# Optimization experiments

Hardware: AMD Instinct MI355X
Metric: run time of the kernel (lower is better)

## Reference

```python
import jax, jax.numpy as jnp
import numpy as np

B, S, H = 2, 2048, 4096
NH, NKV, HD = 32, 8, 128
N_REP = NH // NKV
ROPE_BASE = 10000.0
NEG_INF = -1e9


def setup_inputs() -> dict:
    key = jax.random.key(0)
    k1, k2, k3, k4, k5 = jax.random.split(key, 5)
    hidden_states = jax.random.normal(k1, (B, S, H), dtype=jnp.float32)
    # standard prefill positions 0..S-1 for each batch row
    position_ids = jnp.tile(jnp.arange(S, dtype=jnp.int64)[None, :], (B, 1))
    # additive causal mask, broadcastable over batch and heads
    causal = jnp.tril(jnp.ones((S, S), dtype=bool))
    attention_mask = jnp.where(causal, 0.0, NEG_INF).astype(jnp.float32)[None, None]
    scale = 0.02
    Wq = jax.random.normal(k2, (H, NH * HD), dtype=jnp.float32) * scale
    Wk = jax.random.normal(k3, (H, NKV * HD), dtype=jnp.float32) * scale
    Wv = jax.random.normal(k4, (H, NKV * HD), dtype=jnp.float32) * scale
    Wo = jax.random.normal(k5, (NH * HD, H), dtype=jnp.float32) * scale
    return {"hidden_states": hidden_states, "position_ids": position_ids,
            "attention_mask": attention_mask, "Wq": Wq, "Wk": Wk, "Wv": Wv, "Wo": Wo}


def _rope_cos_sin(position_ids):
    # inv_freq: [HD/2]
    inv_freq = 1.0 / (ROPE_BASE ** (jnp.arange(0, HD, 2, dtype=jnp.float32) / HD))
    freqs = position_ids.astype(jnp.float32)[:, :, None] * inv_freq[None, None, :]  # [B,S,HD/2]
    emb = jnp.concatenate([freqs, freqs], axis=-1)  # [B,S,HD]
    # unsqueeze head dim (unsqueeze_dim=1)
    return jnp.cos(emb)[:, None], jnp.sin(emb)[:, None]  # [B,1,S,HD]


def _rotate_half(x):
    x1, x2 = jnp.split(x, 2, axis=-1)
    return jnp.concatenate([-x2, x1], axis=-1)


def reference(hidden_states, position_ids, attention_mask, Wq, Wk, Wv, Wo):
    b, s, _ = hidden_states.shape
    q = jnp.einsum('bsh,hd->bsd', hidden_states, Wq).reshape(b, s, NH, HD).transpose(0, 2, 1, 3)
    k = jnp.einsum('bsh,hd->bsd', hidden_states, Wk).reshape(b, s, NKV, HD).transpose(0, 2, 1, 3)
    v = jnp.einsum('bsh,hd->bsd', hidden_states, Wv).reshape(b, s, NKV, HD).transpose(0, 2, 1, 3)

    cos, sin = _rope_cos_sin(position_ids)  # [B,1,S,HD]
    q = q * cos + _rotate_half(q) * sin
    k = k * cos + _rotate_half(k) * sin

    # GQA: repeat each kv head N_REP times consecutively -> [B,NH,S,HD]
    k = jnp.repeat(k, N_REP, axis=1)
    v = jnp.repeat(v, N_REP, axis=1)

    scores = jnp.einsum('bhqd,bhkd->bhqk', q, k) / np.sqrt(HD).astype(np.float32)
    scores = scores + attention_mask
    attn = jax.nn.softmax(scores, axis=-1)
    out = jnp.einsum('bhqk,bhkd->bhqd', attn, v)  # [B,NH,S,HD]
    out = out.transpose(0, 2, 1, 3).reshape(b, s, NH * HD)
    return out @ Wo
```

## Files before the change

kernel.cpp:

```cpp
#include <hip/hip_runtime.h>
#include <hip/hip_bf16.h>
#include <stdint.h>
#include <math.h>

#define S_LEN 2048
#define NHEAD 32
#define NKVH  8
#define HDIM  128
#define HID   4096

typedef __attribute__((ext_vector_type(4))) float f32x4;
typedef __attribute__((ext_vector_type(8))) short s16x8;
typedef __attribute__((ext_vector_type(4))) short s16x4;

__device__ __forceinline__ float bf2f(ushort u){
  union { float f; uint32_t i; } c; c.i = ((uint32_t)u) << 16; return c.f;
}
__device__ __forceinline__ ushort f2bf(float f){
  union { float f; uint32_t i; } c; c.f = f;
  uint32_t i = c.i;
  return (ushort)((i + 0x7FFFu + ((i >> 16) & 1u)) >> 16);
}

__global__ void cvtrope_k(const float* __restrict__ src, ushort* __restrict__ dst,
                          float* __restrict__ cost, float* __restrict__ sint){
  int ri = blockIdx.x * 256 + threadIdx.x;
  if (ri < S_LEN * 64){
    int s = ri >> 6, j = ri & 63;
    float invf = powf(10000.0f, -(float)j * (1.0f / 64.0f));
    float a = (float)s * invf;
    cost[ri] = cosf(a);
    sint[ri] = sinf(a);
  }
  size_t i = ((size_t)blockIdx.x * 256 + threadIdx.x) * 8;
  f32x4 a = *(const f32x4*)(src + i);
  f32x4 b = *(const f32x4*)(src + i + 4);
  s16x8 o;
  o[0]=f2bf(a[0]); o[1]=f2bf(a[1]); o[2]=f2bf(a[2]); o[3]=f2bf(a[3]);
  o[4]=f2bf(b[0]); o[5]=f2bf(b[1]); o[6]=f2bf(b[2]); o[7]=f2bf(b[3]);
  *(s16x8*)(dst + i) = o;
}

__device__ __forceinline__ void wtrans_body(const float* __restrict__ W, ushort* __restrict__ WT,
                                            int K, int N, int k0, int n0, int tid){
  __shared__ float T[64][68];
  #pragma unroll
  for (int it = 0; it < 4; ++it){
    int slot = it*256 + tid;
    int kr = slot >> 4, c4 = slot & 15;
    f32x4 v = *(const f32x4*)(W + (size_t)(k0 + kr) * N + n0 + c4*4);
    *(f32x4*)&T[kr][c4*4] = v;
  }
  __syncthreads();
  #pragma unroll
  for (int it = 0; it < 2; ++it){
    int slot = it*256 + tid;
    int nr = slot >> 3, k8 = slot & 7;
    s16x8 o;
    #pragma unroll
    for (int j = 0; j < 8; ++j) o[j] = f2bf(T[k8*8 + j][nr]);
    *(s16x8*)(WT + (size_t)(n0 + nr) * K + k0 + k8*8) = o;
  }
}

__global__ void wtrans4_k(const float* __restrict__ Wq, const float* __restrict__ Wk,
                          const float* __restrict__ Wv, const float* __restrict__ Wo,
                          ushort* __restrict__ WqT, ushort* __restrict__ WkvT,
                          ushort* __restrict__ WoT){
  int y = blockIdx.y;
  const float* W; ushort* WT; int N, n0;
  if (y < 64){ W = Wq; WT = WqT;  N = 4096; n0 = y*64; }
  else if (y < 80){ W = Wk; WT = WkvT; N = 1024; n0 = (y-64)*64; }
  else if (y < 96){ W = Wv; WT = WkvT + (size_t)1024*HID; N = 1024; n0 = (y-80)*64; }
  else { W = Wo; WT = WoT; N = 4096; n0 = (y-96)*64; }
  wtrans_body(W, WT, HID, N, blockIdx.x*64, n0, threadIdx.x);
}

__global__ void vtrans_k(const ushort* __restrict__ KVb, ushort* __restrict__ Vt){
  __shared__ ushort T[64][136];
  int tid = threadIdx.x;
  int s0 = blockIdx.x * 64;
  int bk = blockIdx.y;
  int b = bk >> 3, kvh = bk & 7;
  #pragma unroll
  for (int it = 0; it < 4; ++it){
    int slot = it*256 + tid;
    int sr = slot >> 4, c8 = slot & 15;
    s16x8 v = *(const s16x8*)(KVb + (size_t)(b*S_LEN + s0 + sr) * 2048 + 1024 + kvh*HDIM + c8*8);
    *(s16x8*)&T[sr][c8*8] = v;
  }
  __syncthreads();
  #pragma unroll
  for (int it = 0; it < 4; ++it){
    int slot = it*256 + tid;
    int d = slot >> 3, s8 = slot & 7;
    s16x8 o;
    #pragma unroll
    for (int j = 0; j < 8; ++j) o[j] = (short)T[s8*8 + j][d];
    *(s16x8*)(Vt + ((size_t)bk * HDIM + d) * S_LEN + s0 + s8*8) = o;
  }
}

template<int EPI>
__global__ __launch_bounds__(256)
void gemm_bt(const ushort* __restrict__ A, const ushort* __restrict__ Bt,
             void* __restrict__ Cout, int M, int N, int K,
             const float* __restrict__ cost, const float* __restrict__ sint,
             float oscale)
{
  __shared__ ushort As[128*64];
  __shared__ ushort Bs[128*64];
  const int tid = threadIdx.x;
  const int w = tid >> 6, lane = tid & 63;
  const int l15 = lane & 15, l4 = lane >> 4;
  const size_t Abase = (size_t)blockIdx.x * 128 * K;
  const size_t Bbase = (size_t)blockIdx.y * 128 * K;

  f32x4 acc[2][8] = {};

  const int srow = (w << 3) + (lane >> 3);
  const int scol = (lane & 7) * 8;
  const ushort* Ag = A + Abase + (size_t)srow * K + scol;
  const ushort* Bg = Bt + Bbase + (size_t)srow * K + scol;

  for (int k0 = 0; k0 < K; k0 += 64){
    #pragma unroll
    for (int i = 0; i < 4; ++i){
      __builtin_amdgcn_global_load_lds(
        (const __attribute__((address_space(1))) void*)(Ag + k0 + (size_t)(32*i)*K),
        (__attribute__((address_space(3))) void*)((char*)As + w*1024 + i*4096), 16, 0, 0);
      __builtin_amdgcn_global_load_lds(
        (const __attribute__((address_space(1))) void*)(Bg + k0 + (size_t)(32*i)*K),
        (__attribute__((address_space(3))) void*)((char*)Bs + w*1024 + i*4096), 16, 0, 0);
    }
    __syncthreads();
    #pragma unroll
    for (int kk = 0; kk < 2; ++kk){
      s16x8 af[2], bfr[8];
      #pragma unroll
      for (int m = 0; m < 2; ++m)
        af[m] = *(const s16x8*)&As[(w*32 + m*16 + l15)*64 + kk*32 + l4*8];
      #pragma unroll
      for (int n = 0; n < 8; ++n)
        bfr[n] = *(const s16x8*)&Bs[(n*16 + l15)*64 + kk*32 + l4*8];
      #pragma unroll
      for (int m = 0; m < 2; ++m)
        #pragma unroll
        for (int n = 0; n < 8; ++n)
          acc[m][n] = __builtin_amdgcn_mfma_f32_16x16x32_bf16(af[m], bfr[n], acc[m][n], 0, 0, 0);
    }
    __syncthreads();
  }

  const int r0 = (int)blockIdx.x * 128 + w * 32;
  const int c0 = (int)blockIdx.y * 128;
  if (EPI == 2){
    float* C = (float*)Cout;
    #pragma unroll
    for (int m = 0; m < 2; ++m)
      #pragma unroll
      for (int r = 0; r < 4; ++r){
        size_t rowoff = (size_t)(r0 + m*16 + l4*4 + r) * N + c0;
        #pragma unroll
        for (int n = 0; n < 8; ++n)
          C[rowoff + n*16 + l15] = acc[m][n][r];
      }
  } else if (EPI == 0 || (EPI == 3 && c0 >= 1024)){
    ushort* C = (ushort*)Cout;
    #pragma unroll
    for (int m = 0; m < 2; ++m)
      #pragma unroll
      for (int r = 0; r < 4; ++r){
        size_t rowoff = (size_t)(r0 + m*16 + l4*4 + r) * N + c0;
        #pragma unroll
        for (int n = 0; n < 8; ++n)
          C[rowoff + n*16 + l15] = f2bf(acc[m][n][r]);
      }
  } else {
    ushort* C = (ushort*)Cout;
    #pragma unroll
    for (int m = 0; m < 2; ++m)
      #pragma unroll
      for (int r = 0; r < 4; ++r){
        int row = r0 + m*16 + l4*4 + r;
        int pos = row & (S_LEN - 1);
        size_t rowoff = (size_t)row * N + c0;
        #pragma unroll
        for (int n = 0; n < 4; ++n){
          int d = n*16 + l15;
          float cv = cost[pos*64 + d];
          float sv = sint[pos*64 + d];
          float x1 = acc[m][n][r];
          float x2 = acc[m][n+4][r];
          C[rowoff + d]      = f2bf((x1*cv - x2*sv) * oscale);
          C[rowoff + d + 64] = f2bf((x2*cv + x1*sv) * oscale);
        }
      }
  }
}

template<int EPI>
__global__ __launch_bounds__(512, 2)
void gemm256(const ushort* __restrict__ A, const ushort* __restrict__ Bt,
             void* __restrict__ Cout, int M, int N, int K,
             const float* __restrict__ cost, const float* __restrict__ sint,
             float oscale)
{
  extern __shared__ char L[];
  const int tid = threadIdx.x;
  const int wid = tid >> 6, lane = tid & 63;
  const int wm = wid >> 2, wn = wid & 3;
  const int l15 = lane & 15, l4 = lane >> 4;
  const int swz = (l15 & 7) << 4;
  const int nwg  = gridDim.x;
  const int bid  = blockIdx.x;
  const int sbid = (bid & 7) * (nwg >> 3) + (bid >> 3);
  const int gx   = sbid & 15, gy = sbid >> 4;
  const int brow = gx * 256, bcol = gy * 256;
  const int nt = K >> 6;

  f32x4 acc[8][4] = {};
  s16x8 areg[8], b0reg[4], b1reg[4];

  auto STAGE = [&](int arr, int sh, int bf, int tile){
    int tt = tile < nt ? tile : nt - 1;
    const ushort* gb = arr ? (Bt + (size_t)bcol * K) : (A + (size_t)brow * K);
    char* lb = L + bf*65536 + arr*32768;
    #pragma unroll
    for (int j = 0; j < 2; ++j){
      int c   = j*8 + wid;
      int rg0 = (c >= 8 ? 128 : 0) + sh*64 + ((c*8) & 63);
      int rg  = rg0 + (lane >> 3);
      const char* gsrc = (const char*)(gb + (size_t)rg * K + tt*64)
                       + (((lane & 7) * 16) ^ (((lane >> 3) & 7) << 4));
      __builtin_amdgcn_global_load_lds(
        (const __attribute__((address_space(1))) void*)gsrc,
        (__attribute__((address_space(3))) void*)(lb + rg0*128), 16, 0, 0);
    }
  };
  auto LDA = [&](int bf, int mh){
    const char* ab = L + bf*65536;
    #pragma unroll
    for (int i = 0; i < 4; ++i){
      int row = wm*128 + (mh*4 + i)*16 + l15;
      #pragma unroll
      for (int kk = 0; kk < 2; ++kk)
        areg[i*2+kk] = *(const s16x8*)(ab + row*128 + ((kk*64 + l4*16) ^ swz));
    }
  };
  auto LDB = [&](int bf, int nh, s16x8* breg){
    const char* bb = L + bf*65536 + 32768;
    #pragma unroll
    for (int j = 0; j < 2; ++j){
      int row = wn*64 + (nh*2 + j)*16 + l15;
      #pragma unroll
      for (int kk = 0; kk < 2; ++kk)
        breg[j*2+kk] = *(const s16x8*)(bb + row*128 + ((kk*64 + l4*16) ^ swz));
    }
  };
  auto MFMA16 = [&](int mh, int nh, s16x8* breg){
    __builtin_amdgcn_s_setprio(1);
    #pragma unroll
    for (int kk = 0; kk < 2; ++kk)
      #pragma unroll
      for (int i = 0; i < 4; ++i)
        #pragma unroll
        for (int j = 0; j < 2; ++j)
          acc[mh*4+i][nh*2+j] = __builtin_amdgcn_mfma_f32_16x16x32_bf16(
              areg[i*2+kk], breg[j*2+kk], acc[mh*4+i][nh*2+j], 0, 0, 0);
    __builtin_amdgcn_s_setprio(0);
  };

  STAGE(0,0,0,0); STAGE(1,0,0,0); STAGE(0,1,0,0); STAGE(1,1,0,0);
  STAGE(0,0,1,1); STAGE(1,0,1,1); STAGE(0,1,1,1);
  asm volatile("s_waitcnt vmcnt(6)" ::: "memory");
  __builtin_amdgcn_s_barrier();

  for (int t = 0; t < nt; t += 2){
    LDA(0,0); LDB(0,0,b0reg); STAGE(1,1,1,t+1);
    __builtin_amdgcn_s_barrier();
    MFMA16(0,0,b0reg);
    __builtin_amdgcn_s_barrier();
    LDB(0,1,b1reg); STAGE(0,0,0,t+2);
    __builtin_amdgcn_s_barrier();
    MFMA16(0,1,b1reg);
    __builtin_amdgcn_s_barrier();
    LDA(0,1); STAGE(1,0,0,t+2);
    __builtin_amdgcn_s_barrier();
    MFMA16(1,0,b0reg);
    __builtin_amdgcn_s_barrier();
    STAGE(0,1,0,t+2);
    __builtin_amdgcn_s_barrier();
    MFMA16(1,1,b1reg);
    asm volatile("s_waitcnt vmcnt(6)" ::: "memory");
    __builtin_amdgcn_s_barrier();
    LDA(1,0); LDB(1,0,b0reg); STAGE(1,1,0,t+2);
    __builtin_amdgcn_s_barrier();
    MFMA16(0,0,b0reg);
    __builtin_amdgcn_s_barrier();
    LDB(1,1,b1reg); STAGE(0,0,1,t+3);
    __builtin_amdgcn_s_barrier();
    MFMA16(0,1,b1reg);
    __builtin_amdgcn_s_barrier();
    LDA(1,1); STAGE(1,0,1,t+3);
    __builtin_amdgcn_s_barrier();
    MFMA16(1,0,b0reg);
    __builtin_amdgcn_s_barrier();
    STAGE(0,1,1,t+3);
    __builtin_amdgcn_s_barrier();
    MFMA16(1,1,b1reg);
    asm volatile("s_waitcnt vmcnt(6)" ::: "memory");
    __builtin_amdgcn_s_barrier();
  }
  asm volatile("s_waitcnt vmcnt(0)" ::: "memory");
  __builtin_amdgcn_s_barrier();

  if (EPI == 2){
    float* C = (float*)Cout;
    #pragma unroll
    for (int m = 0; m < 8; ++m)
      #pragma unroll
      for (int r = 0; r < 4; ++r){
        size_t rowoff = (size_t)(brow + wm*128 + m*16 + l4*4 + r) * N + bcol + wn*64;
        #pragma unroll
        for (int n = 0; n < 4; ++n)
          C[rowoff + n*16 + l15] = acc[m][n][r];
      }
  } else {
    float* xls = (float*)L;
    ushort* C = (ushort*)Cout;
    float* mine = xls + wid*2176;
    const float* part = xls + (wid^1)*2176;
    #pragma unroll
    for (int mm = 0; mm < 4; ++mm){
      #pragma unroll
      for (int mi = 0; mi < 2; ++mi){
        int m = mm*2 + mi;
        #pragma unroll
        for (int r = 0; r < 4; ++r)
          #pragma unroll
          for (int n = 0; n < 4; ++n)
            mine[(mi*16 + l4*4 + r)*68 + n*16 + l15] = acc[m][n][r];
      }
      __builtin_amdgcn_s_barrier();
      #pragma unroll
      for (int mi = 0; mi < 2; ++mi){
        int m = mm*2 + mi;
        #pragma unroll
        for (int r = 0; r < 4; ++r){
          int rr = brow + wm*128 + m*16 + l4*4 + r;
          int pos = rr & (S_LEN - 1);
          size_t rowoff = (size_t)rr * N + bcol + wn*64;
          #pragma unroll
          for (int n = 0; n < 4; ++n){
            int d2 = n*16 + l15;
            float x  = acc[m][n][r];
            float px = part[(mi*16 + l4*4 + r)*68 + d2];
            float cv = cost[pos*64 + d2], sv = sint[pos*64 + d2];
            float o = (wn & 1) ? (x*cv + px*sv) : (x*cv - px*sv);
            C[rowoff + d2] = f2bf(o * oscale);
          }
        }
      }
      __builtin_amdgcn_s_barrier();
    }
  }
}

__global__ __launch_bounds__(256, 2)
void attn_k(const ushort* __restrict__ Q, const ushort* __restrict__ KVb,
            const ushort* __restrict__ Vt, ushort* __restrict__ AO)
{
  extern __shared__ char L[];
  const int tid = threadIdx.x, w = tid >> 6, lane = tid & 63;
  const int l15 = lane & 15, l4 = lane >> 4;
  const int swz = (l15 & 7) << 4;

  const int id  = blockIdx.x;
  const int idx = id >> 3;
  const int bk  = (id & 7) * 2 + (idx & 1);
  const int b   = bk >> 3, kvh = bk & 7;
  const int h   = kvh * 4 + ((idx >> 1) & 3);
  const int pair= idx >> 3;

  const char* Kgb = (const char*)(KVb + (size_t)b * S_LEN * 2048 + kvh * HDIM);
  const char* Vgb = (const char*)(Vt + (size_t)bk * HDIM * S_LEN);
  char* pb = L + 65536 + w*4096;

  const int krow_in = lane >> 4;
  const int kbyte   = l15 * 16;
  const int vrow_in = lane >> 3;
  const int vbyte   = (lane & 7) * 16;

  auto STAGE = [&](int kv0, int bf){
    char* kb = L + bf*32768;
    char* vb = kb + 16384;
    #pragma unroll
    for (int i = 0; i < 4; ++i){
      int c = w*4 + i;
      int krow = c*4 + krow_in;
      const char* ksrc = Kgb + (size_t)(kv0 + krow) * 4096 + (kbyte ^ ((krow & 7) << 4));
      __builtin_amdgcn_global_load_lds(
        (const __attribute__((address_space(1))) void*)ksrc,
        (__attribute__((address_space(3))) void*)(kb + c*1024), 16, 0, 0);
      int vrow = c*8 + vrow_in;
      const char* vsrc = Vgb + (size_t)vrow * (S_LEN*2) + kv0*2 + (vbyte ^ ((vrow & 7) << 4));
      __builtin_amdgcn_global_load_lds(
        (const __attribute__((address_space(1))) void*)vsrc,
        (__attribute__((address_space(3))) void*)(vb + c*1024), 16, 0, 0);
    }
  };

  #pragma unroll
  for (int half = 0; half < 2; ++half){
    const int qt  = half ? (15 - pair) : pair;
    const int wq0 = qt * 128 + w * 32;
    const int nt  = 2*qt + 2;

    s16x8 qf[2][4];
    #pragma unroll
    for (int m = 0; m < 2; ++m){
      const ushort* qp = Q + (size_t)(b*S_LEN + wq0 + m*16 + l15) * (NHEAD*HDIM) + h*HDIM + l4*8;
      #pragma unroll
      for (int kk = 0; kk < 4; ++kk)
        qf[m][kk] = *(const s16x8*)(qp + kk*32);
    }

    float mreg0 = -1e30f, mreg1 = -1e30f, lreg0 = 0.f, lreg1 = 0.f;
    f32x4 oacc[2][8] = {};
    const int qlane0 = wq0 + l15, qlane1 = qlane0 + 16;

    int cur = 0;
    STAGE(0, 0);
    __syncthreads();

    for (int t = 0; t < nt; ++t){
      const int kv0 = t * 64;
      if (t + 1 < nt) STAGE(kv0 + 64, cur ^ 1);
      if (kv0 <= wq0 + 31){
        const char* kb = L + cur*32768;
        const char* vb = kb + 16384;
        f32x4 st[4][2] = {};
        #pragma unroll
        for (int kk = 0; kk < 4; ++kk){
          s16x8 kf[4];
          #pragma unroll
          for (int i = 0; i < 4; ++i){
            int row = i*16 + l15;
            kf[i] = *(const s16x8*)(kb + row*256 + ((kk*64 + l4*16) ^ swz));
          }
          __builtin_amdgcn_s_setprio(1);
          #pragma unroll
          for (int i = 0; i < 4; ++i){
            st[i][0] = __builtin_amdgcn_mfma_f32_16x16x32_bf16(kf[i], qf[0][kk], st[i][0], 0, 0, 0);
            st[i][1] = __builtin_amdgcn_mfma_f32_16x16x32_bf16(kf[i], qf[1][kk], st[i][1], 0, 0, 0);
          }
          __builtin_amdgcn_s_setprio(0);
        }
        if (kv0 + 63 > wq0){
          #pragma unroll
          for (int i = 0; i < 4; ++i){
            int kvb = kv0 + i*16 + l4*4;
            #pragma unroll
            for (int r = 0; r < 4; ++r){
              if (kvb + r > qlane0) st[i][0][r] = -1e30f;
              if (kvb + r > qlane1) st[i][1][r] = -1e30f;
            }
          }
        }
        float mx0 = -1e30f, mx1 = -1e30f;
        #pragma unroll
        for (int i = 0; i < 4; ++i){
          mx0 = fmaxf(mx0, fmaxf(fmaxf(st[i][0][0], st[i][0][1]), fmaxf(st[i][0][2], st[i][0][3])));
          mx1 = fmaxf(mx1, fmaxf(fmaxf(st[i][1][0], st[i][1][1]), fmaxf(st[i][1][2], st[i][1][3])));
        }
        mx0 = fmaxf(mx0, __shfl_xor(mx0, 16)); mx0 = fmaxf(mx0, __shfl_xor(mx0, 32));
        mx1 = fmaxf(mx1, __shfl_xor(mx1, 16)); mx1 = fmaxf(mx1, __shfl_xor(mx1, 32));
        bool resc = !__all((mx0 <= mreg0 + 8.0f) & (mx1 <= mreg1 + 8.0f));
        if (resc){
          float mn0 = fmaxf(mreg0, mx0), mn1 = fmaxf(mreg1, mx1);
          float fs0 = __expf(mreg0 - mn0), fs1 = __expf(mreg1 - mn1);
          mreg0 = mn0; mreg1 = mn1; lreg0 *= fs0; lreg1 *= fs1;
          #pragma unroll
          for (int m = 0; m < 2; ++m){
            float fsm = m ? fs1 : fs0;
            #pragma unroll
            for (int r = 0; r < 4; ++r){
              float fb = __shfl(fsm, (lane & 48) | (l4*4 + r));
              #pragma unroll
              for (int n = 0; n < 8; ++n) oacc[m][n][r] *= fb;
            }
          }
        }
        float s0 = 0.f, s1 = 0.f;
        #pragma unroll
        for (int i = 0; i < 4; ++i){
          int col2 = (i*16 + l4*4) * 2;
          f32x4 p0, p1;
          #pragma unroll
          for (int r = 0; r < 4; ++r){
            p0[r] = __expf(st[i][0][r] - mreg0); s0 += p0[r];
            p1[r] = __expf(st[i][1][r] - mreg1); s1 += p1[r];
          }
          s16x4 u0, u1;
          #pragma unroll
          for (int r = 0; r < 4; ++r){ u0[r] = (short)f2bf(p0[r]); u1[r] = (short)f2bf(p1[r]); }
          *(s16x4*)(pb + ((l15*128 + col2) ^ swz))        = u0;
          *(s16x4*)(pb + (((16 + l15)*128 + col2) ^ swz)) = u1;
        }
        lreg0 += s0; lreg1 += s1;
        #pragma unroll
        for (int kk = 0; kk < 2; ++kk){
          s16x8 pf0 = *(const s16x8*)(pb + ((l15*128 + kk*64 + l4*16) ^ swz));
          s16x8 pf1 = *(const s16x8*)(pb + (((16 + l15)*128 + kk*64 + l4*16) ^ swz));
          s16x8 vf[8];
          #pragma unroll
          for (int n = 0; n < 8; ++n){
            int row = n*16 + l15;
            vf[n] = *(const s16x8*)(vb + row*128 + ((kk*64 + l4*16) ^ swz));
          }
          __builtin_amdgcn_s_setprio(1);
          #pragma unroll
          for (int n = 0; n < 8; ++n){
            oacc[0][n] = __builtin_amdgcn_mfma_f32_16x16x32_bf16(pf0, vf[n], oacc[0][n], 0, 0, 0);
            oacc[1][n] = __builtin_amdgcn_mfma_f32_16x16x32_bf16(pf1, vf[n], oacc[1][n], 0, 0, 0);
          }
          __builtin_amdgcn_s_setprio(0);
        }
      }
      __syncthreads();
      cur ^= 1;
    }

    lreg0 += __shfl_xor(lreg0, 16); lreg0 += __shfl_xor(lreg0, 32);
    lreg1 += __shfl_xor(lreg1, 16); lreg1 += __shfl_xor(lreg1, 32);
    float inv0 = 1.0f / lreg0, inv1 = 1.0f / lreg1;
    #pragma unroll
    for (int m = 0; m < 2; ++m){
      float invm = m ? inv1 : inv0;
      #pragma unroll
      for (int r = 0; r < 4; ++r){
        float ib = __shfl(invm, (lane & 48) | (l4*4 + r));
        ushort* dst = AO + (size_t)(b*S_LEN + wq0 + m*16 + l4*4 + r) * (NHEAD*HDIM) + h*HDIM;
        #pragma unroll
        for (int n = 0; n < 8; ++n)
          dst[n*16 + l15] = f2bf(oacc[m][n][r] * ib);
      }
    }
  }
}

extern "C" void kernel_launch(void* const* d_in, const int* in_sizes, int n_in,
                              void* d_out, int out_size, void* d_ws, size_t ws_size,
                              hipStream_t stream)
{
  const float* X  = (const float*)d_in[0];
  const float* Wq = (const float*)d_in[3];
  const float* Wk = (const float*)d_in[4];
  const float* Wv = (const float*)d_in[5];
  const float* Wo = (const float*)d_in[6];

  char* ws = (char*)d_ws;
  float*  cost = (float*) (ws + 0);
  float*  sint = (float*) (ws + 524288);
  ushort* Xb   = (ushort*)(ws + 1048576);
  ushort* WqT  = (ushort*)(ws + 34603008);
  ushort* WkvT = (ushort*)(ws + 68157440);
  ushort* Qb   = (ushort*)(ws + 84934656);
  ushort* KVb  = (ushort*)(ws + 118489088);
  ushort* Vt   = (ushort*)(ws + 135266304);
  ushort* WoT  = (ushort*)(ws + 143654912);
  ushort* AO   = WqT;

  const float qk_scale = 0.08838834764831845f;

  const int GLDS = 131072;
  const int ALDS = 81920;
  hipFuncSetAttribute((const void*)gemm256<1>, hipFuncAttributeMaxDynamicSharedMemorySize, GLDS);
  hipFuncSetAttribute((const void*)gemm256<2>, hipFuncAttributeMaxDynamicSharedMemorySize, GLDS);
  hipFuncSetAttribute((const void*)attn_k,     hipFuncAttributeMaxDynamicSharedMemorySize, ALDS);

  cvtrope_k<<<8192, 256, 0, stream>>>(X, Xb, cost, sint);
  wtrans4_k<<<dim3(64, 160), 256, 0, stream>>>(Wq, Wk, Wv, Wo, WqT, WkvT, WoT);

  gemm256<1><<<256, 512, GLDS, stream>>>(Xb, WqT, Qb, 4096, 4096, 4096, cost, sint, qk_scale);
  gemm_bt<3><<<dim3(32, 16), 256, 0, stream>>>(Xb, WkvT, KVb, 4096, 2048, 4096, cost, sint, 1.0f);

  vtrans_k<<<dim3(32, 16), 256, 0, stream>>>(KVb, Vt);

  attn_k<<<512, 256, ALDS, stream>>>(Qb, KVb, Vt, AO);

  gemm256<2><<<256, 512, GLDS, stream>>>(AO, WoT, d_out, 4096, 4096, 4096, nullptr, nullptr, 1.0f);
}
```

Measured before the change: 506.3 us.

## Merge prep kernels and write transposed V directly from KV GEMM epilogue

```diff
diff --git a/kernel.cpp b/kernel.cpp
--- a/kernel.cpp
+++ b/kernel.cpp
@@ -20,25 +20,6 @@
   union { float f; uint32_t i; } c; c.f = f;
   uint32_t i = c.i;
   return (ushort)((i + 0x7FFFu + ((i >> 16) & 1u)) >> 16);
-}
-
-__global__ void cvtrope_k(const float* __restrict__ src, ushort* __restrict__ dst,
-                          float* __restrict__ cost, float* __restrict__ sint){
-  int ri = blockIdx.x * 256 + threadIdx.x;
-  if (ri < S_LEN * 64){
-    int s = ri >> 6, j = ri & 63;
-    float invf = powf(10000.0f, -(float)j * (1.0f / 64.0f));
-    float a = (float)s * invf;
-    cost[ri] = cosf(a);
-    sint[ri] = sinf(a);
-  }
-  size_t i = ((size_t)blockIdx.x * 256 + threadIdx.x) * 8;
-  f32x4 a = *(const f32x4*)(src + i);
-  f32x4 b = *(const f32x4*)(src + i + 4);
-  s16x8 o;
-  o[0]=f2bf(a[0]); o[1]=f2bf(a[1]); o[2]=f2bf(a[2]); o[3]=f2bf(a[3]);
-  o[4]=f2bf(b[0]); o[5]=f2bf(b[1]); o[6]=f2bf(b[2]); o[7]=f2bf(b[3]);
-  *(s16x8*)(dst + i) = o;
 }
 
 __device__ __forceinline__ void wtrans_body(const float* __restrict__ W, ushort* __restrict__ WT,
@@ -63,41 +44,37 @@
   }
 }
 
-__global__ void wtrans4_k(const float* __restrict__ Wq, const float* __restrict__ Wk,
-                          const float* __restrict__ Wv, const float* __restrict__ Wo,
-                          ushort* __restrict__ WqT, ushort* __restrict__ WkvT,
-                          ushort* __restrict__ WoT){
+__global__ void prep_k(const float* __restrict__ Wq, const float* __restrict__ Wk,
+                       const float* __restrict__ Wv, const float* __restrict__ Wo,
+                       ushort* __restrict__ WqT, ushort* __restrict__ WkvT,
+                       ushort* __restrict__ WoT,
+                       const float* __restrict__ X, ushort* __restrict__ Xb,
+                       float* __restrict__ cost, float* __restrict__ sint){
   int y = blockIdx.y;
-  const float* W; ushort* WT; int N, n0;
-  if (y < 64){ W = Wq; WT = WqT;  N = 4096; n0 = y*64; }
-  else if (y < 80){ W = Wk; WT = WkvT; N = 1024; n0 = (y-64)*64; }
-  else if (y < 96){ W = Wv; WT = WkvT + (size_t)1024*HID; N = 1024; n0 = (y-80)*64; }
-  else { W = Wo; WT = WoT; N = 4096; n0 = (y-96)*64; }
-  wtrans_body(W, WT, HID, N, blockIdx.x*64, n0, threadIdx.x);
-}
-
-__global__ void vtrans_k(const ushort* __restrict__ KVb, ushort* __restrict__ Vt){
-  __shared__ ushort T[64][136];
-  int tid = threadIdx.x;
-  int s0 = blockIdx.x * 64;
-  int bk = blockIdx.y;
-  int b = bk >> 3, kvh = bk & 7;
-  #pragma unroll
-  for (int it = 0; it < 4; ++it){
-    int slot = it*256 + tid;
-    int sr = slot >> 4, c8 = slot & 15;
-    s16x8 v = *(const s16x8*)(KVb + (size_t)(b*S_LEN + s0 + sr) * 2048 + 1024 + kvh*HDIM + c8*8);
-    *(s16x8*)&T[sr][c8*8] = v;
-  }
-  __syncthreads();
-  #pragma unroll
-  for (int it = 0; it < 4; ++it){
-    int slot = it*256 + tid;
-    int d = slot >> 3, s8 = slot & 7;
+  if (y < 160){
+    const float* W; ushort* WT; int N, n0;
+    if (y < 64){ W = Wq; WT = WqT;  N = 4096; n0 = y*64; }
+    else if (y < 80){ W = Wk; WT = WkvT; N = 1024; n0 = (y-64)*64; }
+    else if (y < 96){ W = Wv; WT = WkvT + (size_t)1024*HID; N = 1024; n0 = (y-80)*64; }
+    else { W = Wo; WT = WoT; N = 4096; n0 = (y-96)*64; }
+    wtrans_body(W, WT, HID, N, blockIdx.x*64, n0, threadIdx.x);
+  } else {
+    int cid = (y - 160) * 64 + blockIdx.x;
+    int ri = cid * 256 + threadIdx.x;
+    if (ri < S_LEN * 64){
+      int s = ri >> 6, j = ri & 63;
+      float invf = powf(10000.0f, -(float)j * (1.0f / 64.0f));
+      float a = (float)s * invf;
+      cost[ri] = cosf(a);
+      sint[ri] = sinf(a);
+    }
+    size_t i = ((size_t)cid * 256 + threadIdx.x) * 8;
+    f32x4 a = *(const f32x4*)(X + i);
+    f32x4 b = *(const f32x4*)(X + i + 4);
     s16x8 o;
-    #pragma unroll
-    for (int j = 0; j < 8; ++j) o[j] = (short)T[s8*8 + j][d];
-    *(s16x8*)(Vt + ((size_t)bk * HDIM + d) * S_LEN + s0 + s8*8) = o;
+    o[0]=f2bf(a[0]); o[1]=f2bf(a[1]); o[2]=f2bf(a[2]); o[3]=f2bf(a[3]);
+    o[4]=f2bf(b[0]); o[5]=f2bf(b[1]); o[6]=f2bf(b[2]); o[7]=f2bf(b[3]);
+    *(s16x8*)(Xb + i) = o;
   }
 }
 
@@ -106,7 +83,7 @@
 void gemm_bt(const ushort* __restrict__ A, const ushort* __restrict__ Bt,
              void* __restrict__ Cout, int M, int N, int K,
              const float* __restrict__ cost, const float* __restrict__ sint,
-             float oscale)
+             float oscale, ushort* __restrict__ Vt)
 {
   __shared__ ushort As[128*64];
   __shared__ ushort Bs[128*64];
@@ -165,7 +142,7 @@
         for (int n = 0; n < 8; ++n)
           C[rowoff + n*16 + l15] = acc[m][n][r];
       }
-  } else if (EPI == 0 || (EPI == 3 && c0 >= 1024)){
+  } else if (EPI == 0){
     ushort* C = (ushort*)Cout;
     #pragma unroll
     for (int m = 0; m < 2; ++m)
@@ -175,6 +152,19 @@
         #pragma unroll
         for (int n = 0; n < 8; ++n)
           C[rowoff + n*16 + l15] = f2bf(acc[m][n][r]);
+      }
+  } else if (EPI == 3 && c0 >= 1024){
+    const int kvh = (c0 - 1024) >> 7;
+    #pragma unroll
+    for (int m = 0; m < 2; ++m)
+      #pragma unroll
+      for (int r = 0; r < 4; ++r){
+        int row = r0 + m*16 + l4*4 + r;
+        int b = row >> 11, s = row & (S_LEN - 1);
+        ushort* vbase = Vt + ((size_t)(b*NKVH + kvh) * HDIM) * S_LEN + s;
+        #pragma unroll
+        for (int n = 0; n < 8; ++n)
+          vbase[(size_t)(n*16 + l15) * S_LEN] = f2bf(acc[m][n][r]);
       }
   } else {
     ushort* C = (ushort*)Cout;
@@ -580,13 +570,10 @@
   hipFuncSetAttribute((const void*)gemm256<2>, hipFuncAttributeMaxDynamicSharedMemorySize, GLDS);
   hipFuncSetAttribute((const void*)attn_k,     hipFuncAttributeMaxDynamicSharedMemorySize, ALDS);
 
-  cvtrope_k<<<8192, 256, 0, stream>>>(X, Xb, cost, sint);
-  wtrans4_k<<<dim3(64, 160), 256, 0, stream>>>(Wq, Wk, Wv, Wo, WqT, WkvT, WoT);
+  prep_k<<<dim3(64, 288), 256, 0, stream>>>(Wq, Wk, Wv, Wo, WqT, WkvT, WoT, X, Xb, cost, sint);
 
   gemm256<1><<<256, 512, GLDS, stream>>>(Xb, WqT, Qb, 4096, 4096, 4096, cost, sint, qk_scale);
-  gemm_bt<3><<<dim3(32, 16), 256, 0, stream>>>(Xb, WkvT, KVb, 4096, 2048, 4096, cost, sint, 1.0f);
-
-  vtrans_k<<<dim3(32, 16), 256, 0, stream>>>(KVb, Vt);
+  gemm_bt<3><<<dim3(32, 16), 256, 0, stream>>>(Xb, WkvT, KVb, 4096, 2048, 4096, cost, sint, 1.0f, Vt);
 
   attn_k<<<512, 256, ALDS, stream>>>(Qb, KVb, Vt, AO);
 
```

Result: no change. 501.1 us (-1.0%).
